# Performance work log

Measured on AMD Instinct MI355X. Metric: run time of the kernel, lower is better.

The kernel has to match this reference:

```python
import jax, jax.numpy as jnp
import numpy as np

B, N, F, L = 8, 2048, 128, 2
SLOPE = 0.1  # LeakyReLU negative slope

def lrelu(v):
    return jnp.where(v >= 0, v, SLOPE * v)

def setup_inputs() -> dict:
    key = jax.random.key(0)
    ks = jax.random.split(key, 7)
    scale = 1.0 / np.sqrt(F)
    return {
        "x": jax.random.normal(ks[0], (B, N, F), dtype=jnp.float32),
        "W3": jax.random.normal(ks[1], (L, F, F), dtype=jnp.float32) * scale,
        "b3": jnp.zeros((L, F), dtype=jnp.float32),
        "W4": jax.random.normal(ks[2], (L, F, F), dtype=jnp.float32) * scale,
        "b4": jnp.zeros((L, F), dtype=jnp.float32),
        "W5": jax.random.normal(ks[3], (L, F, F), dtype=jnp.float32) * scale,
        "b5": jnp.zeros((L, F), dtype=jnp.float32),
    }

def reference(x, W3, b3, W4, b4, W5, b5):
    # GraphStack of L GraphLayer modules, mes_type '0':
    #   weight_ij = dot(LeakyReLU(g3(n_i)), LeakyReLU(g4(n_j)))
    #   message_i = mean_{j != i} weight_ij * n_j
    #   n_i_out   = LeakyReLU(g5(message_i)) + n_i
    n = x.shape[1]
    for l in range(W3.shape[0]):
        w1 = lrelu(jnp.einsum('bnf,fg->bng', x, W3[l]) + b3[l])  # [B,N,F]
        w2 = lrelu(jnp.einsum('bnf,fg->bng', x, W4[l]) + b4[l])  # [B,N,F]
        wt = jnp.einsum('bif,bjf->bij', w1, w2)                  # pairwise weights [B,N,N]
        diag = jnp.einsum('bif,bif->bi', w1, w2)                 # self weights to exclude
        msg = (jnp.einsum('bij,bjf->bif', wt, x) - diag[..., None] * x) / (n - 1)
        x = lrelu(jnp.einsum('bif,fg->big', msg, W5[l]) + b5[l]) + x
    return x
```

## Files before the change

kernel.cpp:

```cpp
#include <hip/hip_runtime.h>

#define NN 2048
#define FF 128
#define SLOPE 0.1f
#define LS 136

typedef __attribute__((ext_vector_type(8))) short short8;
typedef __attribute__((ext_vector_type(4))) float f32x4;

__device__ __forceinline__ float lrelu(float v) { return v >= 0.f ? v : SLOPE * v; }

__device__ __forceinline__ ushort f2bf(float f) {
    uint u = __float_as_uint(f);
    return (ushort)((u + 0x7fffu + ((u >> 16) & 1u)) >> 16);
}


__device__ __forceinline__ void mfma_AB(
    const ushort* __restrict__ As, const ushort* __restrict__ Bg,
    int c, int quad, int ct0, f32x4 acc[2][2])
{
#pragma unroll
    for (int kk = 0; kk < 4; kk++) {
        short8 a0 = *(const short8*)&As[c * LS + kk * 32 + quad * 8];
        short8 a1 = *(const short8*)&As[(16 + c) * LS + kk * 32 + quad * 8];
#pragma unroll
        for (int ct = 0; ct < 2; ct++) {
            const int n = (ct0 + ct) * 16 + c;
            short8 bf = *(const short8*)&Bg[n * 128 + kk * 32 + quad * 8];
            acc[0][ct] = __builtin_amdgcn_mfma_f32_16x16x32_bf16(a0, bf, acc[0][ct], 0, 0, 0);
            acc[1][ct] = __builtin_amdgcn_mfma_f32_16x16x32_bf16(a1, bf, acc[1][ct], 0, 0, 0);
        }
    }
}

__device__ __forceinline__ void write_t32(
    const ushort* __restrict__ s, ushort* __restrict__ dstb,
    int jloc0, int tid)
{
    const int g = tid >> 1;
    const int h = tid & 1;
    uint p[8];
#pragma unroll
    for (int jj = 0; jj < 8; jj++) {
        const uint lo = s[(h * 16 + jj * 2) * LS + g];
        const uint hi = s[(h * 16 + jj * 2 + 1) * LS + g];
        p[jj] = lo | (hi << 16);
    }
    uint4* dst = (uint4*)&dstb[(size_t)g * NN + jloc0 + h * 16];
    dst[0] = make_uint4(p[0], p[1], p[2], p[3]);
    dst[1] = make_uint4(p[4], p[5], p[6], p[7]);
}

__device__ __forceinline__ void store_lin32(
    const ushort* __restrict__ s, ushort* __restrict__ g, int tid)
{
#pragma unroll
    for (int i = 0; i < 2; i++) {
        const int off = (i * 256 + tid) * 8;
        *(short8*)&g[off] = *(const short8*)&s[(off >> 7) * LS + (off & 127)];
    }
}

__device__ __forceinline__ void load_lin32(
    const ushort* __restrict__ g, ushort* __restrict__ s, int tid)
{
#pragma unroll
    for (int i = 0; i < 2; i++) {
        const int off = (i * 256 + tid) * 8;
        *(short8*)&s[(off >> 7) * LS + (off & 127)] = *(const short8*)&g[off];
    }
}

__device__ __forceinline__ void epi_w12(
    const f32x4 acc1[2][2], const f32x4 acc2[2][2],
    const float* __restrict__ b3, const float* __restrict__ b4,
    ushort* __restrict__ w1s, ushort* __restrict__ w2s, float* __restrict__ diag_s,
    int c, int quad, int ct0)
{
    float dpar[2][4];
#pragma unroll
    for (int rt = 0; rt < 2; rt++)
#pragma unroll
        for (int r = 0; r < 4; r++) dpar[rt][r] = 0.f;

#pragma unroll
    for (int rt = 0; rt < 2; rt++) {
#pragma unroll
        for (int ct = 0; ct < 2; ct++) {
            const int gcol = (ct0 + ct) * 16 + c;
            const float bb3 = b3[gcol], bb4 = b4[gcol];
#pragma unroll
            for (int r = 0; r < 4; r++) {
                const float v1 = lrelu(acc1[rt][ct][r] + bb3);
                const float v2 = lrelu(acc2[rt][ct][r] + bb4);
                const int lrow = rt * 16 + quad * 4 + r;
                w1s[lrow * LS + gcol] = f2bf(v1);
                w2s[lrow * LS + gcol] = f2bf(v2);
                dpar[rt][r] += v1 * v2;
            }
        }
    }
#pragma unroll
    for (int rt = 0; rt < 2; rt++) {
#pragma unroll
        for (int r = 0; r < 4; r++) {
            float dp = dpar[rt][r];
            dp += __shfl_xor(dp, 1, 64);
            dp += __shfl_xor(dp, 2, 64);
            dp += __shfl_xor(dp, 4, 64);
            dp += __shfl_xor(dp, 8, 64);
            if (c == 0) atomicAdd(&diag_s[rt * 16 + quad * 4 + r], dp);
        }
    }
}

__global__ __launch_bounds__(256) void k_prep(
    const float* __restrict__ W3, const float* __restrict__ W4,
    const float* __restrict__ W5, ushort* __restrict__ Wt)
{
    const int idx = blockIdx.x * 256 + threadIdx.x;
    const int m = idx >> 14;
    const int rem = idx & 16383;
    const int f = rem & 127;
    const int g = rem >> 7;
    const int l = m / 3, w = m % 3;
    const float* src = (w == 0) ? W3 : (w == 1) ? W4 : W5;
    Wt[m * 16384 + g * 128 + f] = f2bf(src[l * 16384 + f * 128 + g]);
}

__global__ __launch_bounds__(256, 2) void k_w12(
    const float* __restrict__ x, const ushort* __restrict__ w3t,
    const ushort* __restrict__ w4t, const float* __restrict__ b3,
    const float* __restrict__ b4, ushort* __restrict__ w1b,
    ushort* __restrict__ w2t, ushort* __restrict__ xt,
    float* __restrict__ diag)
{
    __shared__ ushort xs[32 * LS];
    __shared__ ushort w2s[32 * LS];
    __shared__ float diag_s[32];

    const int tid = threadIdx.x;
    const int row0 = blockIdx.x * 32;
    const int b = row0 >> 11;
    const int jloc0 = row0 & 2047;

    if (tid < 32) diag_s[tid] = 0.f;

    const float4* xg4 = (const float4*)(x + (size_t)row0 * FF);
#pragma unroll
    for (int i = 0; i < 4; i++) {
        const int f4 = i * 256 + tid;
        const int row = f4 >> 5;
        const int k = (f4 & 31) * 4;
        float4 v = xg4[f4];
        ushort4 h;
        h.x = f2bf(v.x); h.y = f2bf(v.y); h.z = f2bf(v.z); h.w = f2bf(v.w);
        *(ushort4*)&xs[row * LS + k] = h;
    }
    __syncthreads();

    write_t32(xs, xt + (size_t)b * (FF * NN), jloc0, tid);

    const int lane = tid & 63;
    const int wave = tid >> 6;
    const int c = lane & 15;
    const int quad = lane >> 4;
    const int ct0 = wave * 2;

    f32x4 a1[2][2], a2[2][2];
#pragma unroll
    for (int rt = 0; rt < 2; rt++)
#pragma unroll
        for (int ct = 0; ct < 2; ct++) { a1[rt][ct] = (f32x4)0.f; a2[rt][ct] = (f32x4)0.f; }
    mfma_AB(xs, w3t, c, quad, ct0, a1);
    mfma_AB(xs, w4t, c, quad, ct0, a2);

    __syncthreads();
    epi_w12(a1, a2, b3, b4, xs, w2s, diag_s, c, quad, ct0);
    __syncthreads();

    store_lin32(xs, w1b + (size_t)row0 * FF, tid);
    write_t32(w2s, w2t + (size_t)b * (FF * NN), jloc0, tid);
    if (tid < 32) diag[row0 + tid] = diag_s[tid];
}

__global__ __launch_bounds__(256, 2) void k_S(
    const ushort* __restrict__ xt, const ushort* __restrict__ w2t,
    ushort* __restrict__ St)
{
    __shared__ float red[4][256];
    const int tid = threadIdx.x;
    const int lane = tid & 63;
    const int wave = tid >> 6;
    const int c = lane & 15;
    const int quad = lane >> 4;

    const int sb = blockIdx.x >> 6;
    const int gq = (blockIdx.x >> 3) & 7;
    const int fs = blockIdx.x & 7;

    const int j0 = wave * 512 + quad * 8;
    const ushort* ap = &xt[(size_t)sb * (FF * NN) + (size_t)(gq * 16 + c) * NN + j0];
    const ushort* bp = &w2t[(size_t)sb * (FF * NN) + (size_t)(fs * 16 + c) * NN + j0];

    f32x4 acc = (f32x4)0.f;
#pragma unroll
    for (int it = 0; it < 16; it++) {
        short8 a = *(const short8*)(ap + it * 32);
        short8 bv = *(const short8*)(bp + it * 32);
        acc = __builtin_amdgcn_mfma_f32_16x16x32_bf16(a, bv, acc, 0, 0, 0);
    }
#pragma unroll
    for (int r = 0; r < 4; r++) red[wave][(quad * 4 + r) * 16 + c] = acc[r];
    __syncthreads();

    const float s = red[0][tid] + red[1][tid] + red[2][tid] + red[3][tid];
    const int gl = tid >> 4, fl = tid & 15;
    St[(size_t)sb * (FF * FF) + (size_t)(gq * 16 + gl) * FF + fs * 16 + fl] = f2bf(s);
}

__global__ __launch_bounds__(256, 2) void k_out(
    const float* __restrict__ xin, const ushort* __restrict__ w1b,
    const ushort* __restrict__ St, const float* __restrict__ diag,
    const ushort* __restrict__ w5t, const float* __restrict__ b5,
    float* __restrict__ out)
{
    __shared__ ushort sW[32 * LS];
    __shared__ ushort sT[32 * LS];

    const int tid = threadIdx.x;
    const int row0 = blockIdx.x * 32;
    const int b = row0 >> 11;
    const ushort* Sb = St + (size_t)b * (FF * FF);

    load_lin32(w1b + (size_t)row0 * FF, sW, tid);
    __syncthreads();

    const int lane = tid & 63;
    const int wave = tid >> 6;
    const int c = lane & 15;
    const int quad = lane >> 4;
    const int ct0 = wave * 2;

    f32x4 accm[2][2];
#pragma unroll
    for (int rt = 0; rt < 2; rt++)
#pragma unroll
        for (int ct = 0; ct < 2; ct++) accm[rt][ct] = (f32x4)0.f;
    mfma_AB(sW, Sb, c, quad, ct0, accm);

    const float inv = 1.f / (float)(NN - 1);
    float xsv[2][2][4];
#pragma unroll
    for (int rt = 0; rt < 2; rt++) {
        float dg[4];
#pragma unroll
        for (int r = 0; r < 4; r++) dg[r] = diag[row0 + rt * 16 + quad * 4 + r];
#pragma unroll
        for (int ct = 0; ct < 2; ct++) {
            const int gcol = (ct0 + ct) * 16 + c;
#pragma unroll
            for (int r = 0; r < 4; r++) {
                const int lrow = rt * 16 + quad * 4 + r;
                const float xv = xin[(size_t)(row0 + lrow) * FF + gcol];
                xsv[rt][ct][r] = xv;
                sT[lrow * LS + gcol] = f2bf((accm[rt][ct][r] - dg[r] * xv) * inv);
            }
        }
    }
    __syncthreads();

    f32x4 acc2[2][2];
#pragma unroll
    for (int rt = 0; rt < 2; rt++)
#pragma unroll
        for (int ct = 0; ct < 2; ct++) acc2[rt][ct] = (f32x4)0.f;
    mfma_AB(sT, w5t, c, quad, ct0, acc2);

#pragma unroll
    for (int rt = 0; rt < 2; rt++) {
#pragma unroll
        for (int ct = 0; ct < 2; ct++) {
            const int gcol = (ct0 + ct) * 16 + c;
            const float bb = b5[gcol];
#pragma unroll
            for (int r = 0; r < 4; r++) {
                const int lrow = rt * 16 + quad * 4 + r;
                out[(size_t)(row0 + lrow) * FF + gcol] =
                    lrelu(acc2[rt][ct][r] + bb) + xsv[rt][ct][r];
            }
        }
    }
}

__global__ __launch_bounds__(256, 2) void k_out_w12(
    const float* __restrict__ x, const ushort* __restrict__ w1b_in,
    const ushort* __restrict__ St, const float* __restrict__ diag_in,
    const ushort* __restrict__ w5t, const float* __restrict__ b5,
    float* __restrict__ out,
    const ushort* __restrict__ w3t, const ushort* __restrict__ w4t,
    const float* __restrict__ b3, const float* __restrict__ b4,
    ushort* __restrict__ w1b, ushort* __restrict__ w2t,
    ushort* __restrict__ xt, float* __restrict__ diag)
{
    __shared__ ushort sA[32 * LS];
    __shared__ ushort sB[32 * LS];
    __shared__ float diag_s[32];

    const int tid = threadIdx.x;
    const int row0 = blockIdx.x * 32;
    const int b = row0 >> 11;
    const int jloc0 = row0 & 2047;
    const ushort* Sb = St + (size_t)b * (FF * FF);

    if (tid < 32) diag_s[tid] = 0.f;

    load_lin32(w1b_in + (size_t)row0 * FF, sA, tid);
    __syncthreads();

    const int lane = tid & 63;
    const int wave = tid >> 6;
    const int c = lane & 15;
    const int quad = lane >> 4;
    const int ct0 = wave * 2;

    f32x4 accm[2][2];
#pragma unroll
    for (int rt = 0; rt < 2; rt++)
#pragma unroll
        for (int ct = 0; ct < 2; ct++) accm[rt][ct] = (f32x4)0.f;
    mfma_AB(sA, Sb, c, quad, ct0, accm);

    const float inv = 1.f / (float)(NN - 1);
    float xsv[2][2][4];
#pragma unroll
    for (int rt = 0; rt < 2; rt++) {
        float dg[4];
#pragma unroll
        for (int r = 0; r < 4; r++) dg[r] = diag_in[row0 + rt * 16 + quad * 4 + r];
#pragma unroll
        for (int ct = 0; ct < 2; ct++) {
            const int gcol = (ct0 + ct) * 16 + c;
#pragma unroll
            for (int r = 0; r < 4; r++) {
                const int lrow = rt * 16 + quad * 4 + r;
                const float xv = x[(size_t)(row0 + lrow) * FF + gcol];
                xsv[rt][ct][r] = xv;
                sB[lrow * LS + gcol] = f2bf((accm[rt][ct][r] - dg[r] * xv) * inv);
            }
        }
    }
    __syncthreads();

    f32x4 acc2[2][2];
#pragma unroll
    for (int rt = 0; rt < 2; rt++)
#pragma unroll
        for (int ct = 0; ct < 2; ct++) acc2[rt][ct] = (f32x4)0.f;
    mfma_AB(sB, w5t, c, quad, ct0, acc2);

#pragma unroll
    for (int rt = 0; rt < 2; rt++) {
#pragma unroll
        for (int ct = 0; ct < 2; ct++) {
            const int gcol = (ct0 + ct) * 16 + c;
            const float bb = b5[gcol];
#pragma unroll
            for (int r = 0; r < 4; r++) {
                const int lrow = rt * 16 + quad * 4 + r;
                const float ov = lrelu(acc2[rt][ct][r] + bb) + xsv[rt][ct][r];
                out[(size_t)(row0 + lrow) * FF + gcol] = ov;
                sA[lrow * LS + gcol] = f2bf(ov);
            }
        }
    }
    __syncthreads();

    write_t32(sA, xt + (size_t)b * (FF * NN), jloc0, tid);

    f32x4 a1[2][2], a2[2][2];
#pragma unroll
    for (int rt = 0; rt < 2; rt++)
#pragma unroll
        for (int ct = 0; ct < 2; ct++) { a1[rt][ct] = (f32x4)0.f; a2[rt][ct] = (f32x4)0.f; }
    mfma_AB(sA, w3t, c, quad, ct0, a1);
    mfma_AB(sA, w4t, c, quad, ct0, a2);

    __syncthreads();
    epi_w12(a1, a2, b3, b4, sB , sA , diag_s, c, quad, ct0);
    __syncthreads();

    store_lin32(sB, w1b + (size_t)row0 * FF, tid);
    write_t32(sA, w2t + (size_t)b * (FF * NN), jloc0, tid);
    if (tid < 32) diag[row0 + tid] = diag_s[tid];
}

extern "C" void kernel_launch(void* const* d_in, const int* in_sizes, int n_in,
                              void* d_out, int out_size, void* d_ws, size_t ws_size,
                              hipStream_t stream)
{
    const float* x  = (const float*)d_in[0];
    const float* W3 = (const float*)d_in[1];
    const float* b3 = (const float*)d_in[2];
    const float* W4 = (const float*)d_in[3];
    const float* b4 = (const float*)d_in[4];
    const float* W5 = (const float*)d_in[5];
    const float* b5 = (const float*)d_in[6];
    float* out = (float*)d_out;

    char* ws = (char*)d_ws;
    ushort* w1b  = (ushort*)(ws);
    ushort* w2t  = (ushort*)(ws + ((size_t)4  << 20));
    ushort* xt   = (ushort*)(ws + ((size_t)8  << 20));
    float*  diag = (float*) (ws + ((size_t)12 << 20));
    ushort* St   = (ushort*)(ws + ((size_t)13 << 20));
    ushort* Wt   = (ushort*)(ws + ((size_t)13 << 20) + (512 << 10));

    k_prep<<<384, 256, 0, stream>>>(W3, W4, W5, Wt);
    k_w12<<<512, 256, 0, stream>>>(x, Wt, Wt + 16384, b3, b4, w1b, w2t, xt, diag);
    k_S<<<512, 256, 0, stream>>>(xt, w2t, St);
    k_out_w12<<<512, 256, 0, stream>>>(x, w1b, St, diag, Wt + 2 * 16384, b5, out,
                                       Wt + 3 * 16384, Wt + 4 * 16384,
                                       b3 + FF, b4 + FF, w1b, w2t, xt, diag);
    k_S<<<512, 256, 0, stream>>>(xt, w2t, St);
    k_out<<<512, 256, 0, stream>>>(out, w1b, St, diag, Wt + 5 * 16384, b5 + FF, out);
}
```

Baseline: 125.1 us.

## Fold weight prep kernel into k_w12 with per-block LDS weight conversion

Removes the separate k_prep launch. Each k_w12 block now converts W3 and W4 from fp32 into a transposed bf16 LDS buffer and runs the MFMAs from LDS. The blocks also write the bf16 transposes for the remaining weight matrices (W5 and layer 2) that later kernels read. This saves one kernel launch and its dependency, but every block repeats the weight conversion and re-reads 128 KB of weights, and a 34 KB LDS buffer plus two extra barriers may limit occupancy.

```diff
diff --git a/kernel.cpp b/kernel.cpp
--- a/kernel.cpp
+++ b/kernel.cpp
@@ -16,22 +16,29 @@
 }
 
 
+__device__ __forceinline__ void mfma_AB_s(
+    const ushort* __restrict__ As, const ushort* __restrict__ Bs, int bs,
+    int c, int quad, int ct0, f32x4 acc[2][2])
+{
+#pragma unroll
+    for (int kk = 0; kk < 4; kk++) {
+        short8 a0 = *(const short8*)&As[c * LS + kk * 32 + quad * 8];
+        short8 a1 = *(const short8*)&As[(16 + c) * LS + kk * 32 + quad * 8];
+#pragma unroll
+        for (int ct = 0; ct < 2; ct++) {
+            const int n = (ct0 + ct) * 16 + c;
+            short8 bf = *(const short8*)&Bs[n * bs + kk * 32 + quad * 8];
+            acc[0][ct] = __builtin_amdgcn_mfma_f32_16x16x32_bf16(a0, bf, acc[0][ct], 0, 0, 0);
+            acc[1][ct] = __builtin_amdgcn_mfma_f32_16x16x32_bf16(a1, bf, acc[1][ct], 0, 0, 0);
+        }
+    }
+}
+
 __device__ __forceinline__ void mfma_AB(
     const ushort* __restrict__ As, const ushort* __restrict__ Bg,
     int c, int quad, int ct0, f32x4 acc[2][2])
 {
-#pragma unroll
-    for (int kk = 0; kk < 4; kk++) {
-        short8 a0 = *(const short8*)&As[c * LS + kk * 32 + quad * 8];
-        short8 a1 = *(const short8*)&As[(16 + c) * LS + kk * 32 + quad * 8];
-#pragma unroll
-        for (int ct = 0; ct < 2; ct++) {
-            const int n = (ct0 + ct) * 16 + c;
-            short8 bf = *(const short8*)&Bg[n * 128 + kk * 32 + quad * 8];
-            acc[0][ct] = __builtin_amdgcn_mfma_f32_16x16x32_bf16(a0, bf, acc[0][ct], 0, 0, 0);
-            acc[1][ct] = __builtin_amdgcn_mfma_f32_16x16x32_bf16(a1, bf, acc[1][ct], 0, 0, 0);
-        }
-    }
+    mfma_AB_s(As, Bg, 128, c, quad, ct0, acc);
 }
 
 __device__ __forceinline__ void write_t32(
@@ -69,6 +76,22 @@
     for (int i = 0; i < 2; i++) {
         const int off = (i * 256 + tid) * 8;
         *(short8*)&s[(off >> 7) * LS + (off & 127)] = *(const short8*)&g[off];
+    }
+}
+
+__device__ __forceinline__ void conv_wt(
+    const float* __restrict__ W, ushort* __restrict__ wbuf, int tid)
+{
+#pragma unroll
+    for (int i = 0; i < 16; i++) {
+        const int i4 = i * 256 + tid;
+        const int f = i4 >> 5;
+        const int g0 = (i4 & 31) * 4;
+        const float4 v = ((const float4*)W)[i4];
+        wbuf[(g0 + 0) * LS + f] = f2bf(v.x);
+        wbuf[(g0 + 1) * LS + f] = f2bf(v.y);
+        wbuf[(g0 + 2) * LS + f] = f2bf(v.z);
+        wbuf[(g0 + 3) * LS + f] = f2bf(v.w);
     }
 }
 
@@ -115,29 +138,17 @@
     }
 }
 
-__global__ __launch_bounds__(256) void k_prep(
+__global__ __launch_bounds__(256, 2) void k_w12(
+    const float* __restrict__ x,
     const float* __restrict__ W3, const float* __restrict__ W4,
-    const float* __restrict__ W5, ushort* __restrict__ Wt)
-{
-    const int idx = blockIdx.x * 256 + threadIdx.x;
-    const int m = idx >> 14;
-    const int rem = idx & 16383;
-    const int f = rem & 127;
-    const int g = rem >> 7;
-    const int l = m / 3, w = m % 3;
-    const float* src = (w == 0) ? W3 : (w == 1) ? W4 : W5;
-    Wt[m * 16384 + g * 128 + f] = f2bf(src[l * 16384 + f * 128 + g]);
-}
-
-__global__ __launch_bounds__(256, 2) void k_w12(
-    const float* __restrict__ x, const ushort* __restrict__ w3t,
-    const ushort* __restrict__ w4t, const float* __restrict__ b3,
-    const float* __restrict__ b4, ushort* __restrict__ w1b,
-    ushort* __restrict__ w2t, ushort* __restrict__ xt,
-    float* __restrict__ diag)
+    const float* __restrict__ W5,
+    const float* __restrict__ b3, const float* __restrict__ b4,
+    ushort* __restrict__ w1b, ushort* __restrict__ w2t, ushort* __restrict__ xt,
+    float* __restrict__ diag, ushort* __restrict__ Wt)
 {
     __shared__ ushort xs[32 * LS];
     __shared__ ushort w2s[32 * LS];
+    __shared__ ushort wbuf[128 * LS];
     __shared__ float diag_s[32];
 
     const int tid = threadIdx.x;
@@ -146,6 +157,18 @@
     const int jloc0 = row0 & 2047;
 
     if (tid < 32) diag_s[tid] = 0.f;
+
+    {
+        const int idx = blockIdx.x * 256 + tid;
+        if (idx < 4 * 16384) {
+            const int m = (idx >> 14) + 2;
+            const int rem = idx & 16383;
+            const int f = rem & 127, g = rem >> 7;
+            const int l = m / 3, w = m % 3;
+            const float* src = (w == 0) ? W3 : (w == 1) ? W4 : W5;
+            Wt[m * 16384 + g * 128 + f] = f2bf(src[l * 16384 + f * 128 + g]);
+        }
+    }
 
     const float4* xg4 = (const float4*)(x + (size_t)row0 * FF);
 #pragma unroll
@@ -158,6 +181,7 @@
         h.x = f2bf(v.x); h.y = f2bf(v.y); h.z = f2bf(v.z); h.w = f2bf(v.w);
         *(ushort4*)&xs[row * LS + k] = h;
     }
+    conv_wt(W3, wbuf, tid);
     __syncthreads();
 
     write_t32(xs, xt + (size_t)b * (FF * NN), jloc0, tid);
@@ -173,8 +197,12 @@
     for (int rt = 0; rt < 2; rt++)
 #pragma unroll
         for (int ct = 0; ct < 2; ct++) { a1[rt][ct] = (f32x4)0.f; a2[rt][ct] = (f32x4)0.f; }
-    mfma_AB(xs, w3t, c, quad, ct0, a1);
-    mfma_AB(xs, w4t, c, quad, ct0, a2);
+
+    mfma_AB_s(xs, wbuf, LS, c, quad, ct0, a1);
+    __syncthreads();
+    conv_wt(W4, wbuf, tid);
+    __syncthreads();
+    mfma_AB_s(xs, wbuf, LS, c, quad, ct0, a2);
 
     __syncthreads();
     epi_w12(a1, a2, b3, b4, xs, w2s, diag_s, c, quad, ct0);
@@ -417,8 +445,7 @@
     ushort* St   = (ushort*)(ws + ((size_t)13 << 20));
     ushort* Wt   = (ushort*)(ws + ((size_t)13 << 20) + (512 << 10));
 
-    k_prep<<<384, 256, 0, stream>>>(W3, W4, W5, Wt);
-    k_w12<<<512, 256, 0, stream>>>(x, Wt, Wt + 16384, b3, b4, w1b, w2t, xt, diag);
+    k_w12<<<512, 256, 0, stream>>>(x, W3, W4, W5, b3, b4, w1b, w2t, xt, diag, Wt);
     k_S<<<512, 256, 0, stream>>>(xt, w2t, St);
     k_out_w12<<<512, 256, 0, stream>>>(x, w1b, St, diag, Wt + 2 * 16384, b5, out,
                                        Wt + 3 * 16384, Wt + 4 * 16384,
```

Measured after the change: 135.9 us. 8.6% more time.
